# Kernel optimization log

Measured on AMD Instinct MI355X. Metric: run time of the kernel, lower is better.

Reference implementation:

```python
import jax, jax.numpy as jnp
import numpy as np

N = 100_000
E = 1_600_000
F_IN, D1, D2, D_EMB = 64, 32, 64, 64
NUM_GRAPHS = 16
BN_EPS = 1e-5


def _glorot(key, shape):
    fan_in, fan_out = shape[0], shape[1]
    lim = (6.0 / (fan_in + fan_out)) ** 0.5
    return jax.random.uniform(key, shape, jnp.float32, -lim, lim)


def setup_inputs() -> dict:
    key = jax.random.key(0)
    ks = jax.random.split(key, 12)
    x = jax.random.normal(ks[0], (N, F_IN), jnp.float32)
    edge_index = jax.random.randint(ks[1], (2, E), 0, N, jnp.int64)
    batch = jnp.sort(jax.random.randint(ks[2], (N,), 0, NUM_GRAPHS, jnp.int64))
    return {
        "x": x,
        "edge_index": edge_index,
        "batch": batch,
        "num_graphs": NUM_GRAPHS,
        "num_nodes": N,
        "W1a": _glorot(ks[3], (F_IN, D1)), "b1a": jnp.zeros((D1,), jnp.float32),
        "W1b": _glorot(ks[4], (D1, D2)), "b1b": jnp.zeros((D2,), jnp.float32),
        "g1": jnp.ones((D2,), jnp.float32), "be1": jnp.zeros((D2,), jnp.float32),
        "W2a": _glorot(ks[5], (D2, D2)), "b2a": jnp.zeros((D2,), jnp.float32),
        "W2b": _glorot(ks[6], (D2, D_EMB)), "b2b": jnp.zeros((D_EMB,), jnp.float32),
        "g2": jnp.ones((D_EMB,), jnp.float32), "be2": jnp.zeros((D_EMB,), jnp.float32),
    }


def _batchnorm_train(h, gamma, beta):
    mean = jnp.mean(h, axis=0)
    var = jnp.mean(jnp.square(h - mean), axis=0)  # biased var, as torch BN uses for normalization
    return (h - mean) * jax.lax.rsqrt(var + BN_EPS) * gamma + beta


def _gin_aggregate(x, src, dst, valid, n_nodes):
    # sum_{j in N(i)} x_j over valid edges only (masked scatter-add)
    msg = x[src] * valid[:, None]  # [E, D]
    return jax.ops.segment_sum(msg, dst, num_segments=n_nodes)


def reference(x, edge_index, batch, num_graphs, num_nodes,
              W1a, b1a, W1b, b1b, g1, be1,
              W2a, b2a, W2b, b2b, g2, be2):
    n_edges = edge_index.shape[1]
    per = n_edges // num_graphs
    # edge_mask: per-edge threshold g * num_nodes / num_graphs applied to both rows
    thresh = jnp.repeat(jnp.arange(num_graphs), per).astype(jnp.float32) * (num_nodes / num_graphs)
    valid = jnp.all(edge_index.astype(jnp.float32) - thresh[None, :] >= 0.0, axis=0)
    valid = valid.astype(x.dtype)
    src, dst = edge_index[0], edge_index[1]

    # GINConv 1 (eps=0): nn1(x + aggr)
    h = x + _gin_aggregate(x, src, dst, valid, num_nodes)
    h = jax.nn.relu(h @ W1a + b1a) @ W1b + b1b
    h = jax.nn.relu(h)
    h = _batchnorm_train(h, g1, be1)

    # GINConv 2
    h = h + _gin_aggregate(h, src, dst, valid, num_nodes)
    h = jax.nn.relu(h @ W2a + b2a) @ W2b + b2b
    h = jax.nn.relu(h)
    h = _batchnorm_train(h, g2, be2)

    # global_mean_pool
    sums = jax.ops.segment_sum(h, batch, num_segments=num_graphs)
    counts = jax.ops.segment_sum(jnp.ones((h.shape[0],), h.dtype), batch, num_segments=num_graphs)
    return sums / jnp.maximum(counts, 1.0)[:, None]
```

## Files before the change

kernel.cpp:

```cpp
#include <hip/hip_runtime.h>
#include <hip/hip_fp16.h>

#define NG 16
#define D 64
#define SLOT 32
#define INP 68
#define NPB 64

union HF4 { float4 f4; __half2 h2[4]; };
union HF2 { float2 f2; __half2 h2[2]; };

__global__ void to_half_kernel(const float* __restrict__ in,
                               float2* __restrict__ out, int n4,
                               float4* __restrict__ xz,
                               float4* __restrict__ hz) {
  int t = blockIdx.x * 256 + threadIdx.x;
  if (blockIdx.x == 0 && threadIdx.x < 16) {
    float4 z = make_float4(0.f, 0.f, 0.f, 0.f);
    if (threadIdx.x < 8) xz[threadIdx.x] = z;
    else hz[threadIdx.x - 8] = z;
  }
  if (t < n4) {
    float4 v = ((const float4*)in)[t];
    HF2 u;
    u.h2[0] = __floats2half2_rn(v.x, v.y);
    u.h2[1] = __floats2half2_rn(v.z, v.w);
    out[t] = u.f2;
  }
}

__global__ void build_csr_kernel(const int* __restrict__ ei,
                                 int* __restrict__ fill,
                                 int* __restrict__ col,
                                 int E, int per, int tmul) {
  int e = blockIdx.x * blockDim.x + threadIdx.x;
  if (e >= E) return;
  int src = ei[e];
  int dst = ei[E + e];
  int g = e / per;
  int thr = g * tmul;
  if (src >= thr && dst >= thr) {
    int k = atomicAdd(&fill[dst], 1);
    if (k < SLOT) col[dst * SLOT + k] = src;
  }
}

__device__ __forceinline__ void tree_reduce_2x32(float* s_in, int tid) {
#pragma unroll
  for (int s = 16; s >= 1; s >>= 1) {
    if (tid < 32 * s) {
      int h = tid / (16 * s);
      int r = (tid / 16) % s;
      int qq = tid & 15;
      float4* a = (float4*)&s_in[(h * 32 + r) * INP + qq * 4];
      const float4 b = *(const float4*)&s_in[(h * 32 + r + s) * INP + qq * 4];
      a->x += b.x; a->y += b.y; a->z += b.z; a->w += b.w;
    }
    __syncthreads();
  }
}

template <int MID, bool FOLD_BN, int EPI>
__global__ __launch_bounds__(512, 2) void fused_layer_kernel(
    const float4* __restrict__ feat4,
    const int* __restrict__ col, const int* __restrict__ deg,
    const float* __restrict__ bn_sum, const float* __restrict__ bn_sq,
    const float* __restrict__ bn_gamma, const float* __restrict__ bn_beta,
    float invN,
    const float* __restrict__ Wa, const float* __restrict__ ba,
    const float* __restrict__ Wb, const float* __restrict__ bb,
    float2* __restrict__ out2,
    const int* __restrict__ batch,
    float* __restrict__ st_sum,
    float* __restrict__ st_sq,
    float* __restrict__ cnt,
    int N) {
  __shared__ float s_in[NPB * INP];
  __shared__ __half s_Wa[D * MID];
  __shared__ __half s_Wb[MID * D];
  __shared__ float s_bna[FOLD_BN ? D : 1];
  __shared__ float s_bnb[FOLD_BN ? D : 1];
  __shared__ int s_cnt[2];

  int tid = threadIdx.x;

  {
    const float4* wa4 = (const float4*)Wa;
    const float4* wb4 = (const float4*)Wb;
    __half2* sa2 = (__half2*)s_Wa;
    __half2* sb2 = (__half2*)s_Wb;
    constexpr int NW = D * MID / 4;
#pragma unroll
    for (int i = tid; i < NW; i += 512) {
      float4 a = wa4[i];
      float4 b = wb4[i];
      sa2[2 * i + 0] = __floats2half2_rn(a.x, a.y);
      sa2[2 * i + 1] = __floats2half2_rn(a.z, a.w);
      sb2[2 * i + 0] = __floats2half2_rn(b.x, b.y);
      sb2[2 * i + 1] = __floats2half2_rn(b.z, b.w);
    }
  }
  if (FOLD_BN && tid < D) {
    float mean = bn_sum[tid] * invN;
    float var = bn_sq[tid] * invN - mean * mean;
    float av = bn_gamma[tid] * rsqrtf(var + 1e-5f);
    s_bna[tid] = av;
    s_bnb[tid] = bn_beta[tid] - mean * av;
  }
  if (EPI == 2 && tid < 2) s_cnt[tid] = 0;
  __syncthreads();

  int base = blockIdx.x * NPB;

  {
    int slot = tid >> 3;
    int q8 = tid & 7;
    int node = base + slot;
    if (node < N) {
      int d = min(deg[node], SLOT);
      const int* cl = col + node * SLOT;
      float acc[8];
      {
        HF4 s; s.f4 = feat4[(size_t)node * 8 + q8];
#pragma unroll
        for (int i = 0; i < 4; i++) {
          float2 f = __half22float2(s.h2[i]);
          acc[2 * i] = f.x; acc[2 * i + 1] = f.y;
        }
      }
      int dpad = (d + 7) & ~7;
      for (int j = 0; j < dpad; j += 8) {
        int4 sa = *(const int4*)(cl + j);
        int4 sb = *(const int4*)(cl + j + 4);
        int i0 = (j + 0 < d) ? sa.x : N;
        int i1 = (j + 1 < d) ? sa.y : N;
        int i2 = (j + 2 < d) ? sa.z : N;
        int i3 = (j + 3 < d) ? sa.w : N;
        int i4 = (j + 4 < d) ? sb.x : N;
        int i5 = (j + 5 < d) ? sb.y : N;
        int i6 = (j + 6 < d) ? sb.z : N;
        int i7 = (j + 7 < d) ? sb.w : N;
        HF4 u0, u1, u2, u3, u4, u5, u6, u7;
        u0.f4 = feat4[(size_t)i0 * 8 + q8];
        u1.f4 = feat4[(size_t)i1 * 8 + q8];
        u2.f4 = feat4[(size_t)i2 * 8 + q8];
        u3.f4 = feat4[(size_t)i3 * 8 + q8];
        u4.f4 = feat4[(size_t)i4 * 8 + q8];
        u5.f4 = feat4[(size_t)i5 * 8 + q8];
        u6.f4 = feat4[(size_t)i6 * 8 + q8];
        u7.f4 = feat4[(size_t)i7 * 8 + q8];
#pragma unroll
        for (int i = 0; i < 4; i++) {
          float2 f0 = __half22float2(u0.h2[i]), f1 = __half22float2(u1.h2[i]);
          float2 f2 = __half22float2(u2.h2[i]), f3 = __half22float2(u3.h2[i]);
          float2 f4 = __half22float2(u4.h2[i]), f5 = __half22float2(u5.h2[i]);
          float2 f6 = __half22float2(u6.h2[i]), f7 = __half22float2(u7.h2[i]);
          acc[2 * i]     += (f0.x + f1.x + f2.x + f3.x) + (f4.x + f5.x + f6.x + f7.x);
          acc[2 * i + 1] += (f0.y + f1.y + f2.y + f3.y) + (f4.y + f5.y + f6.y + f7.y);
        }
      }
      if (FOLD_BN) {
        float dp = (float)(d + 1);
        int c = q8 * 8;
#pragma unroll
        for (int i = 0; i < 8; i++)
          acc[i] = s_bna[c + i] * acc[i] + dp * s_bnb[c + i];
      }
      *(float4*)&s_in[slot * INP + q8 * 8] =
          make_float4(acc[0], acc[1], acc[2], acc[3]);
      *(float4*)&s_in[slot * INP + q8 * 8 + 4] =
          make_float4(acc[4], acc[5], acc[6], acc[7]);
    }
  }
  __syncthreads();

  int q = tid & 15;
  int r2 = tid >> 4;
  int n0 = 2 * r2, n1 = n0 + 1;
  int node0 = base + n0, node1 = base + n1;
  constexpr int C1 = MID / 16;
  float4 o0, o1;
  {
    float acc0[C1], acc1[C1];
#pragma unroll
    for (int u = 0; u < C1; u++) { acc0[u] = ba[q * C1 + u]; acc1[u] = acc0[u]; }
#pragma unroll 4
    for (int j = 0; j < D; j++) {
      float v0 = s_in[n0 * INP + j];
      float v1 = s_in[n1 * INP + j];
      if constexpr (C1 == 2) {
        float2 w = __half22float2(((const __half2*)s_Wa)[j * 16 + q]);
        acc0[0] += v0 * w.x; acc0[1] += v0 * w.y;
        acc1[0] += v1 * w.x; acc1[1] += v1 * w.y;
      } else {
        HF2 u; u.f2 = ((const float2*)s_Wa)[j * 16 + q];
        float2 wA = __half22float2(u.h2[0]);
        float2 wB = __half22float2(u.h2[1]);
        acc0[0] += v0 * wA.x; acc0[1] += v0 * wA.y;
        acc0[2] += v0 * wB.x; acc0[3] += v0 * wB.y;
        acc1[0] += v1 * wA.x; acc1[1] += v1 * wA.y;
        acc1[2] += v1 * wB.x; acc1[3] += v1 * wB.y;
      }
    }
#pragma unroll
    for (int u = 0; u < C1; u++) {
      acc0[u] = fmaxf(acc0[u], 0.f);
      acc1[u] = fmaxf(acc1[u], 0.f);
    }

    o0 = *(const float4*)(bb + q * 4);
    o1 = o0;
#pragma unroll 8
    for (int k = 0; k < MID; k++) {
      float m0 = __shfl(acc0[k % C1], k / C1, 16);
      float m1 = __shfl(acc1[k % C1], k / C1, 16);
      HF2 u; u.f2 = ((const float2*)s_Wb)[k * 16 + q];
      float2 wA = __half22float2(u.h2[0]);
      float2 wB = __half22float2(u.h2[1]);
      o0.x += m0 * wA.x; o0.y += m0 * wA.y; o0.z += m0 * wB.x; o0.w += m0 * wB.y;
      o1.x += m1 * wA.x; o1.y += m1 * wA.y; o1.z += m1 * wB.x; o1.w += m1 * wB.y;
    }
    o0.x = fmaxf(o0.x, 0.f); o0.y = fmaxf(o0.y, 0.f);
    o0.z = fmaxf(o0.z, 0.f); o0.w = fmaxf(o0.w, 0.f);
    o1.x = fmaxf(o1.x, 0.f); o1.y = fmaxf(o1.y, 0.f);
    o1.z = fmaxf(o1.z, 0.f); o1.w = fmaxf(o1.w, 0.f);
    if (EPI == 1) {
      if (node0 < N) {
        HF2 u;
        u.h2[0] = __floats2half2_rn(o0.x, o0.y);
        u.h2[1] = __floats2half2_rn(o0.z, o0.w);
        out2[(size_t)node0 * 16 + q] = u.f2;
      }
      if (node1 < N) {
        HF2 u;
        u.h2[0] = __floats2half2_rn(o1.x, o1.y);
        u.h2[1] = __floats2half2_rn(o1.z, o1.w);
        out2[(size_t)node1 * 16 + q] = u.f2;
      }
    }
    if (node0 >= N) o0 = make_float4(0.f, 0.f, 0.f, 0.f);
    if (node1 >= N) o1 = make_float4(0.f, 0.f, 0.f, 0.f);
  }

  if (EPI == 1) {
    __syncthreads();
    *(float4*)&s_in[r2 * INP + q * 4] =
        make_float4(o0.x + o1.x, o0.y + o1.y, o0.z + o1.z, o0.w + o1.w);
    *(float4*)&s_in[(32 + r2) * INP + q * 4] =
        make_float4(o0.x * o0.x + o1.x * o1.x, o0.y * o0.y + o1.y * o1.y,
                    o0.z * o0.z + o1.z * o1.z, o0.w * o0.w + o1.w * o1.w);
    __syncthreads();
    tree_reduce_2x32(s_in, tid);
    if (tid < D) {
      atomicAdd(&st_sum[tid], s_in[tid]);
      atomicAdd(&st_sq[tid], s_in[32 * INP + tid]);
    }
  }

  if (EPI == 2) {
    int b0 = (node0 < N) ? batch[node0] : -1;
    int b1 = (node1 < N) ? batch[node1] : -1;
    int g_lo = batch[base];
    int g_hi = batch[min(base + NPB - 1, N - 1)];

    __syncthreads();
    if (q == 0) {
      atomicAdd(&s_cnt[0], (b0 == g_lo ? 1 : 0) + (b1 == g_lo ? 1 : 0));
      if (g_hi != g_lo)
        atomicAdd(&s_cnt[1], (b0 == g_hi ? 1 : 0) + (b1 == g_hi ? 1 : 0));
    }

    float w0 = (b0 == g_lo) ? 1.f : 0.f;
    float w1 = (b1 == g_lo) ? 1.f : 0.f;
    *(float4*)&s_in[r2 * INP + q * 4] =
        make_float4(w0 * o0.x + w1 * o1.x, w0 * o0.y + w1 * o1.y,
                    w0 * o0.z + w1 * o1.z, w0 * o0.w + w1 * o1.w);
    *(float4*)&s_in[(32 + r2) * INP + q * 4] =
        make_float4(o0.x * o0.x + o1.x * o1.x, o0.y * o0.y + o1.y * o1.y,
                    o0.z * o0.z + o1.z * o1.z, o0.w * o0.w + o1.w * o1.w);
    __syncthreads();
    tree_reduce_2x32(s_in, tid);
    if (tid < D) {
      atomicAdd(&st_sum[g_lo * D + tid], s_in[tid]);
      atomicAdd(&st_sq[tid], s_in[32 * INP + tid]);
    }
    if (tid == 0) atomicAdd(&cnt[g_lo], (float)s_cnt[0]);

    if (g_hi != g_lo) {
      __syncthreads();
      float u0 = (b0 == g_hi) ? 1.f : 0.f;
      float u1 = (b1 == g_hi) ? 1.f : 0.f;
      *(float4*)&s_in[r2 * INP + q * 4] =
          make_float4(u0 * o0.x + u1 * o1.x, u0 * o0.y + u1 * o1.y,
                      u0 * o0.z + u1 * o1.z, u0 * o0.w + u1 * o1.w);
      *(float4*)&s_in[(32 + r2) * INP + q * 4] = make_float4(0.f, 0.f, 0.f, 0.f);
      __syncthreads();
      tree_reduce_2x32(s_in, tid);
      if (tid < D) atomicAdd(&st_sum[g_hi * D + tid], s_in[tid]);
      if (tid == 0) atomicAdd(&cnt[g_hi], (float)s_cnt[1]);
    }
  }
}

__global__ void final_kernel(const float* __restrict__ pool,
                             const float* __restrict__ cnt,
                             const float* __restrict__ sq,
                             const float* __restrict__ gamma,
                             const float* __restrict__ beta,
                             float invN, float* __restrict__ out) {
  int c = threadIdx.x;
  float s = 0.f;
#pragma unroll
  for (int g = 0; g < NG; g++) s += pool[g * D + c];
  float mean = s * invN;
  float var = sq[c] * invN - mean * mean;
  float a = gamma[c] * rsqrtf(var + 1e-5f);
  float b = beta[c] - mean * a;
#pragma unroll
  for (int g = 0; g < NG; g++) {
    float n = cnt[g];
    out[g * D + c] = (a * pool[g * D + c] + n * b) / fmaxf(n, 1.f);
  }
}

extern "C" void kernel_launch(void* const* d_in, const int* in_sizes, int n_in,
                              void* d_out, int out_size, void* d_ws, size_t ws_size,
                              hipStream_t stream) {
  const float* x   = (const float*)d_in[0];
  const int* ei    = (const int*)d_in[1];
  const int* batch = (const int*)d_in[2];
  const float* W1a = (const float*)d_in[5];
  const float* b1a = (const float*)d_in[6];
  const float* W1b = (const float*)d_in[7];
  const float* b1b = (const float*)d_in[8];
  const float* g1  = (const float*)d_in[9];
  const float* be1 = (const float*)d_in[10];
  const float* W2a = (const float*)d_in[11];
  const float* b2a = (const float*)d_in[12];
  const float* W2b = (const float*)d_in[13];
  const float* b2b = (const float*)d_in[14];
  const float* g2  = (const float*)d_in[15];
  const float* be2 = (const float*)d_in[16];

  int N = in_sizes[0] / D;
  int E = in_sizes[1] / 2;
  int per = E / NG;
  int tmul = N / NG;
  float invN = 1.f / (float)N;

  float* ws = (float*)d_ws;
  size_t ndh = (size_t)(N + 1) * D / 2;
  float* h1h = ws;
  float* xh  = ws + ndh;
  int*   col = (int*)(ws + 2 * ndh);
  float* stats = ws + 2 * ndh + (size_t)N * SLOT;
  float* sum1 = stats;
  float* sq1  = stats + 64;
  float* pool = stats + 128;
  float* cnt  = stats + 128 + NG * D;
  float* sq2  = stats + 144 + NG * D;
  int*   fill = (int*)(stats + 208 + NG * D);

  hipMemsetAsync(stats, 0, (208 + NG * D + N) * sizeof(float), stream);

  int n4 = N * D / 4;
  to_half_kernel<<<(n4 + 255) / 256, 256, 0, stream>>>(
      x, (float2*)xh, n4,
      (float4*)(xh + (size_t)N * D / 2),
      (float4*)(h1h + (size_t)N * D / 2));

  build_csr_kernel<<<(E + 255) / 256, 256, 0, stream>>>(ei, fill, col, E, per, tmul);

  int fblocks = (N + NPB - 1) / NPB;

  fused_layer_kernel<32, false, 1><<<fblocks, 512, 0, stream>>>(
      (const float4*)xh, col, fill, nullptr, nullptr, nullptr, nullptr, invN,
      W1a, b1a, W1b, b1b, (float2*)h1h, nullptr, sum1, sq1, nullptr, N);

  fused_layer_kernel<64, true, 2><<<fblocks, 512, 0, stream>>>(
      (const float4*)h1h, col, fill, sum1, sq1, g1, be1, invN,
      W2a, b2a, W2b, b2b, nullptr, batch, pool, sq2, cnt, N);

  final_kernel<<<1, 64, 0, stream>>>(pool, cnt, sq2, g2, be2, invN, (float*)d_out);
}
```

Measured before the change: 264.3 us.

## Merge fp16 conversion with CSR build and vectorize gather/MLP math with float2 FMA

Combines the fp16 conversion kernel and the CSR-building kernel into one prep launch, which saves a launch and lets the two independent streams of work overlap. The neighbor gather now handles 16 neighbors per iteration instead of 8, putting more loads in flight, and accumulates in float2 so the compiler can emit packed FP32 adds. The two MLP matmuls are rewritten with float2 FMA helpers to encourage packed v_pk_fma instructions. The cost is higher register pressure from 16 outstanding HF4 loads and more padded dummy loads for nodes with low degree.

New measurement: 248.6 us. -5.9%, faster.

```diff
diff --git a/kernel.cpp b/kernel.cpp
--- a/kernel.cpp
+++ b/kernel.cpp
@@ -10,10 +10,19 @@
 union HF4 { float4 f4; __half2 h2[4]; };
 union HF2 { float2 f2; __half2 h2[2]; };
 
-__global__ void to_half_kernel(const float* __restrict__ in,
-                               float2* __restrict__ out, int n4,
-                               float4* __restrict__ xz,
-                               float4* __restrict__ hz) {
+__device__ __forceinline__ float2 f2fma(float2 a, float2 b, float2 c) {
+  return make_float2(fmaf(a.x, b.x, c.x), fmaf(a.y, b.y, c.y));
+}
+__device__ __forceinline__ float2 f2add(float2 a, float2 b) {
+  return make_float2(a.x + b.x, a.y + b.y);
+}
+
+__global__ void prep_kernel(const float* __restrict__ x,
+                            float2* __restrict__ xh, int n4,
+                            float4* __restrict__ xz, float4* __restrict__ hz,
+                            const int* __restrict__ ei,
+                            int* __restrict__ fill, int* __restrict__ col,
+                            int E, int per, int tmul) {
   int t = blockIdx.x * 256 + threadIdx.x;
   if (blockIdx.x == 0 && threadIdx.x < 16) {
     float4 z = make_float4(0.f, 0.f, 0.f, 0.f);
@@ -21,27 +30,20 @@
     else hz[threadIdx.x - 8] = z;
   }
   if (t < n4) {
-    float4 v = ((const float4*)in)[t];
+    float4 v = ((const float4*)x)[t];
     HF2 u;
     u.h2[0] = __floats2half2_rn(v.x, v.y);
     u.h2[1] = __floats2half2_rn(v.z, v.w);
-    out[t] = u.f2;
-  }
-}
-
-__global__ void build_csr_kernel(const int* __restrict__ ei,
-                                 int* __restrict__ fill,
-                                 int* __restrict__ col,
-                                 int E, int per, int tmul) {
-  int e = blockIdx.x * blockDim.x + threadIdx.x;
-  if (e >= E) return;
-  int src = ei[e];
-  int dst = ei[E + e];
-  int g = e / per;
-  int thr = g * tmul;
-  if (src >= thr && dst >= thr) {
-    int k = atomicAdd(&fill[dst], 1);
-    if (k < SLOT) col[dst * SLOT + k] = src;
+    xh[t] = u.f2;
+  }
+  if (t < E) {
+    int src = ei[t];
+    int dst = ei[E + t];
+    int thr = (t / per) * tmul;
+    if (src >= thr && dst >= thr) {
+      int k = atomicAdd(&fill[dst], 1);
+      if (k < SLOT) col[dst * SLOT + k] = src;
+    }
   }
 }
 
@@ -119,57 +121,51 @@
     if (node < N) {
       int d = min(deg[node], SLOT);
       const int* cl = col + node * SLOT;
-      float acc[8];
+      float2 acc[4];
       {
         HF4 s; s.f4 = feat4[(size_t)node * 8 + q8];
 #pragma unroll
-        for (int i = 0; i < 4; i++) {
-          float2 f = __half22float2(s.h2[i]);
-          acc[2 * i] = f.x; acc[2 * i + 1] = f.y;
-        }
-      }
-      int dpad = (d + 7) & ~7;
-      for (int j = 0; j < dpad; j += 8) {
+        for (int i = 0; i < 4; i++) acc[i] = __half22float2(s.h2[i]);
+      }
+      int dpad = (d + 15) & ~15;
+      for (int j = 0; j < dpad; j += 16) {
         int4 sa = *(const int4*)(cl + j);
         int4 sb = *(const int4*)(cl + j + 4);
-        int i0 = (j + 0 < d) ? sa.x : N;
-        int i1 = (j + 1 < d) ? sa.y : N;
-        int i2 = (j + 2 < d) ? sa.z : N;
-        int i3 = (j + 3 < d) ? sa.w : N;
-        int i4 = (j + 4 < d) ? sb.x : N;
-        int i5 = (j + 5 < d) ? sb.y : N;
-        int i6 = (j + 6 < d) ? sb.z : N;
-        int i7 = (j + 7 < d) ? sb.w : N;
-        HF4 u0, u1, u2, u3, u4, u5, u6, u7;
-        u0.f4 = feat4[(size_t)i0 * 8 + q8];
-        u1.f4 = feat4[(size_t)i1 * 8 + q8];
-        u2.f4 = feat4[(size_t)i2 * 8 + q8];
-        u3.f4 = feat4[(size_t)i3 * 8 + q8];
-        u4.f4 = feat4[(size_t)i4 * 8 + q8];
-        u5.f4 = feat4[(size_t)i5 * 8 + q8];
-        u6.f4 = feat4[(size_t)i6 * 8 + q8];
-        u7.f4 = feat4[(size_t)i7 * 8 + q8];
-#pragma unroll
-        for (int i = 0; i < 4; i++) {
-          float2 f0 = __half22float2(u0.h2[i]), f1 = __half22float2(u1.h2[i]);
-          float2 f2 = __half22float2(u2.h2[i]), f3 = __half22float2(u3.h2[i]);
-          float2 f4 = __half22float2(u4.h2[i]), f5 = __half22float2(u5.h2[i]);
-          float2 f6 = __half22float2(u6.h2[i]), f7 = __half22float2(u7.h2[i]);
-          acc[2 * i]     += (f0.x + f1.x + f2.x + f3.x) + (f4.x + f5.x + f6.x + f7.x);
-          acc[2 * i + 1] += (f0.y + f1.y + f2.y + f3.y) + (f4.y + f5.y + f6.y + f7.y);
+        int4 sc = *(const int4*)(cl + j + 8);
+        int4 sd = *(const int4*)(cl + j + 12);
+        int idx[16];
+        idx[0]  = (j + 0  < d) ? sa.x : N;  idx[1]  = (j + 1  < d) ? sa.y : N;
+        idx[2]  = (j + 2  < d) ? sa.z : N;  idx[3]  = (j + 3  < d) ? sa.w : N;
+        idx[4]  = (j + 4  < d) ? sb.x : N;  idx[5]  = (j + 5  < d) ? sb.y : N;
+        idx[6]  = (j + 6  < d) ? sb.z : N;  idx[7]  = (j + 7  < d) ? sb.w : N;
+        idx[8]  = (j + 8  < d) ? sc.x : N;  idx[9]  = (j + 9  < d) ? sc.y : N;
+        idx[10] = (j + 10 < d) ? sc.z : N;  idx[11] = (j + 11 < d) ? sc.w : N;
+        idx[12] = (j + 12 < d) ? sd.x : N;  idx[13] = (j + 13 < d) ? sd.y : N;
+        idx[14] = (j + 14 < d) ? sd.z : N;  idx[15] = (j + 15 < d) ? sd.w : N;
+        HF4 u[16];
+#pragma unroll
+        for (int i = 0; i < 16; i++) u[i].f4 = feat4[(size_t)idx[i] * 8 + q8];
+#pragma unroll
+        for (int i = 0; i < 16; i++) {
+#pragma unroll
+          for (int c = 0; c < 4; c++)
+            acc[c] = f2add(acc[c], __half22float2(u[i].h2[c]));
         }
       }
       if (FOLD_BN) {
         float dp = (float)(d + 1);
-        int c = q8 * 8;
-#pragma unroll
-        for (int i = 0; i < 8; i++)
-          acc[i] = s_bna[c + i] * acc[i] + dp * s_bnb[c + i];
+        int c0 = q8 * 8;
+#pragma unroll
+        for (int c = 0; c < 4; c++) {
+          float2 a2 = *(const float2*)&s_bna[c0 + 2 * c];
+          float2 b2 = *(const float2*)&s_bnb[c0 + 2 * c];
+          acc[c] = f2fma(a2, acc[c], make_float2(dp * b2.x, dp * b2.y));
+        }
       }
       *(float4*)&s_in[slot * INP + q8 * 8] =
-          make_float4(acc[0], acc[1], acc[2], acc[3]);
+          make_float4(acc[0].x, acc[0].y, acc[1].x, acc[1].y);
       *(float4*)&s_in[slot * INP + q8 * 8 + 4] =
-          make_float4(acc[4], acc[5], acc[6], acc[7]);
+          make_float4(acc[2].x, acc[2].y, acc[3].x, acc[3].y);
     }
   }
   __syncthreads();
@@ -179,51 +175,60 @@
   int n0 = 2 * r2, n1 = n0 + 1;
   int node0 = base + n0, node1 = base + n1;
   constexpr int C1 = MID / 16;
+  constexpr int C2 = C1 / 2;
   float4 o0, o1;
   {
-    float acc0[C1], acc1[C1];
-#pragma unroll
-    for (int u = 0; u < C1; u++) { acc0[u] = ba[q * C1 + u]; acc1[u] = acc0[u]; }
+    float2 acc0[C2], acc1[C2];
+#pragma unroll
+    for (int u = 0; u < C2; u++) {
+      acc0[u] = *(const float2*)&ba[q * C1 + 2 * u];
+      acc1[u] = acc0[u];
+    }
 #pragma unroll 4
     for (int j = 0; j < D; j++) {
-      float v0 = s_in[n0 * INP + j];
-      float v1 = s_in[n1 * INP + j];
+      float2 v0 = make_float2(s_in[n0 * INP + j], s_in[n0 * INP + j]);
+      float2 v1 = make_float2(s_in[n1 * INP + j], s_in[n1 * INP + j]);
       if constexpr (C1 == 2) {
         float2 w = __half22float2(((const __half2*)s_Wa)[j * 16 + q]);
-        acc0[0] += v0 * w.x; acc0[1] += v0 * w.y;
-        acc1[0] += v1 * w.x; acc1[1] += v1 * w.y;
+        acc0[0] = f2fma(v0, w, acc0[0]);
+        acc1[0] = f2fma(v1, w, acc1[0]);
       } else {
         HF2 u; u.f2 = ((const float2*)s_Wa)[j * 16 + q];
         float2 wA = __half22float2(u.h2[0]);
         float2 wB = __half22float2(u.h2[1]);
-        acc0[0] += v0 * wA.x; acc0[1] += v0 * wA.y;
-        acc0[2] += v0 * wB.x; acc0[3] += v0 * wB.y;
-        acc1[0] += v1 * wA.x; acc1[1] += v1 * wA.y;
-        acc1[2] += v1 * wB.x; acc1[3] += v1 * wB.y;
-      }
-    }
-#pragma unroll
-    for (int u = 0; u < C1; u++) {
-      acc0[u] = fmaxf(acc0[u], 0.f);
-      acc1[u] = fmaxf(acc1[u], 0.f);
-    }
-
-    o0 = *(const float4*)(bb + q * 4);
-    o1 = o0;
+        acc0[0] = f2fma(v0, wA, acc0[0]);
+        acc0[1] = f2fma(v0, wB, acc0[1]);
+        acc1[0] = f2fma(v1, wA, acc1[0]);
+        acc1[1] = f2fma(v1, wB, acc1[1]);
+      }
+    }
+#pragma unroll
+    for (int u = 0; u < C2; u++) {
+      acc0[u].x = fmaxf(acc0[u].x, 0.f); acc0[u].y = fmaxf(acc0[u].y, 0.f);
+      acc1[u].x = fmaxf(acc1[u].x, 0.f); acc1[u].y = fmaxf(acc1[u].y, 0.f);
+    }
+
+    float2 o0a = *(const float2*)&bb[q * 4];
+    float2 o0b = *(const float2*)&bb[q * 4 + 2];
+    float2 o1a = o0a, o1b = o0b;
 #pragma unroll 8
     for (int k = 0; k < MID; k++) {
-      float m0 = __shfl(acc0[k % C1], k / C1, 16);
-      float m1 = __shfl(acc1[k % C1], k / C1, 16);
+      float s0 = ((k % C1) & 1) ? acc0[(k % C1) >> 1].y : acc0[(k % C1) >> 1].x;
+      float s1 = ((k % C1) & 1) ? acc1[(k % C1) >> 1].y : acc1[(k % C1) >> 1].x;
+      float m0 = __shfl(s0, k / C1, 16);
+      float m1 = __shfl(s1, k / C1, 16);
       HF2 u; u.f2 = ((const float2*)s_Wb)[k * 16 + q];
       float2 wA = __half22float2(u.h2[0]);
       float2 wB = __half22float2(u.h2[1]);
-      o0.x += m0 * wA.x; o0.y += m0 * wA.y; o0.z += m0 * wB.x; o0.w += m0 * wB.y;
-      o1.x += m1 * wA.x; o1.y += m1 * wA.y; o1.z += m1 * wB.x; o1.w += m1 * wB.y;
-    }
-    o0.x = fmaxf(o0.x, 0.f); o0.y = fmaxf(o0.y, 0.f);
-    o0.z = fmaxf(o0.z, 0.f); o0.w = fmaxf(o0.w, 0.f);
-    o1.x = fmaxf(o1.x, 0.f); o1.y = fmaxf(o1.y, 0.f);
-    o1.z = fmaxf(o1.z, 0.f); o1.w = fmaxf(o1.w, 0.f);
+      float2 m0f = make_float2(m0, m0);
+      float2 m1f = make_float2(m1, m1);
+      o0a = f2fma(m0f, wA, o0a); o0b = f2fma(m0f, wB, o0b);
+      o1a = f2fma(m1f, wA, o1a); o1b = f2fma(m1f, wB, o1b);
+    }
+    o0 = make_float4(fmaxf(o0a.x, 0.f), fmaxf(o0a.y, 0.f),
+                     fmaxf(o0b.x, 0.f), fmaxf(o0b.y, 0.f));
+    o1 = make_float4(fmaxf(o1a.x, 0.f), fmaxf(o1a.y, 0.f),
+                     fmaxf(o1b.x, 0.f), fmaxf(o1b.y, 0.f));
     if (EPI == 1) {
       if (node0 < N) {
         HF2 u;
@@ -364,12 +369,12 @@
   hipMemsetAsync(stats, 0, (208 + NG * D + N) * sizeof(float), stream);
 
   int n4 = N * D / 4;
-  to_half_kernel<<<(n4 + 255) / 256, 256, 0, stream>>>(
+  int pgrid = (max(n4, E) + 255) / 256;
+  prep_kernel<<<pgrid, 256, 0, stream>>>(
       x, (float2*)xh, n4,
       (float4*)(xh + (size_t)N * D / 2),
-      (float4*)(h1h + (size_t)N * D / 2));
-
-  build_csr_kernel<<<(E + 255) / 256, 256, 0, stream>>>(ei, fill, col, E, per, tmul);
+      (float4*)(h1h + (size_t)N * D / 2),
+      ei, fill, col, E, per, tmul);
 
   int fblocks = (N + NPB - 1) / NPB;
 
```
